# Kernel tuning notes

Measured on AMD Instinct MI355X. Metric: run time of the kernel, lower is better.

## Reference

```python
import math
import jax, jax.numpy as jnp
import numpy as np

B, V, F, H, W = 1, 2, 4, 16, 28
TPF = H * W            # 448 tokens per frame
VS = F * TPF           # 1792 tokens per view
TS = V * VS            # 3584 total tokens
DIM, NH = 1536, 12
HD = DIM // NH         # 128
EPS = 1e-6
SCALE = 1.0 / math.sqrt(HD)


def _rope_angle_table(max_len=1024):
    # Wan-style 3D rope: head_dim//2 = 64 channels split [22, 21, 21] for (f, h, w)
    parts = []
    for full in (44, 42, 42):
        inv = 1.0 / (10000.0 ** (np.arange(0, full, 2) / full))
        parts.append(np.outer(np.arange(max_len), inv))
    return np.concatenate(parts, axis=1).astype(np.float32)  # [max_len, 64]


def setup_inputs():
    key = jax.random.key(0)
    ks = jax.random.split(key, 6)
    p = lambda k, shp: 0.02 * jax.random.normal(k, shp, dtype=jnp.float32)
    return {
        "x": jax.random.normal(ks[0], (B, TS, DIM), dtype=jnp.float32),
        "freqs": jnp.asarray(_rope_angle_table()),
        "q_w": p(ks[1], (DIM, DIM)), "q_b": jnp.zeros((DIM,), jnp.float32),
        "k_w": p(ks[2], (DIM, DIM)), "k_b": jnp.zeros((DIM,), jnp.float32),
        "v_w": p(ks[3], (DIM, DIM)), "v_b": jnp.zeros((DIM,), jnp.float32),
        "o_w": p(ks[4], (DIM, DIM)), "o_b": jnp.zeros((DIM,), jnp.float32),
        "norm_q_w": jnp.ones((DIM,), jnp.float32),
        "norm_k_w": jnp.ones((DIM,), jnp.float32),
        "seq_lens": jnp.full((B,), TS, jnp.int32),
        "view_grid_sizes": jnp.broadcast_to(jnp.array([F, H, W], jnp.int32), (B, V, 3)),
        "view_seq_lens": jnp.full((B, V), VS, jnp.int32),
        "total_seq_lens": jnp.full((B,), TS, jnp.int32),
    }


def _rms_norm(x, w):
    x32 = x.astype(jnp.float32)
    y = x32 * jax.lax.rsqrt(jnp.mean(x32 * x32, axis=-1, keepdims=True) + EPS)
    return y.astype(x.dtype) * w


def _rope_angles(freqs):
    c = HD // 2                                   # 64
    s0, s1 = c - 2 * (c // 3), c // 3             # 22, 21
    af = jnp.broadcast_to(freqs[:F, None, None, :s0], (F, H, W, s0))
    ah = jnp.broadcast_to(freqs[None, :H, None, s0:s0 + s1], (F, H, W, s1))
    aw = jnp.broadcast_to(freqs[None, None, :W, s0 + s1:c], (F, H, W, c - s0 - s1))
    return jnp.concatenate([af, ah, aw], axis=-1).reshape(VS, c)  # [VS, 64]


def _apply_rope(x, ang):
    # x: [N, S, NH, HD]; pairs are (x[..., 2i], x[..., 2i+1]) as in view_as_complex
    cos = jnp.cos(ang)[None, :, None, :]
    sin = jnp.sin(ang)[None, :, None, :]
    xr = x.reshape(x.shape[:-1] + (HD // 2, 2))
    r0 = xr[..., 0] * cos - xr[..., 1] * sin
    r1 = xr[..., 0] * sin + xr[..., 1] * cos
    return jnp.stack([r0, r1], axis=-1).reshape(x.shape)


def _attn_lse(q, k, v):
    # q,k,v: [N, S, NH, HD] -> out [N, S, NH, HD], lse [N, S, NH]
    logits = jnp.einsum('bqhd,bkhd->bhqk', q, k) * SCALE
    lse = jax.nn.logsumexp(logits, axis=-1)       # [N, NH, Sq]
    p = jnp.exp(logits - lse[..., None])
    out = jnp.einsum('bhqk,bkhd->bqhd', p, v)
    return out, jnp.transpose(lse, (0, 2, 1))


def _forward(x, freqs, q_w, q_b, k_w, k_b, v_w, v_b, o_w, o_b, norm_q_w, norm_k_w):
    xv = x[:, :TS]
    q = _rms_norm(xv @ q_w.T + q_b, norm_q_w)
    k = _rms_norm(xv @ k_w.T + k_b, norm_k_w)
    v = xv @ v_w.T + v_b
    q = q.reshape(B * V, VS, NH, HD)
    k = k.reshape(B * V, VS, NH, HD)
    v = v.reshape(B * V, VS, NH, HD)
    ang = _rope_angles(freqs)
    q = _apply_rope(q, ang)
    k = _apply_rope(k, ang)
    # intra-view attention over the full view sequence
    out_i, lse_i = _attn_lse(q, k, v)
    # cross-view per-frame attention: swap the two views for K/V
    k_sw = k.reshape(B, V, F, TPF, NH, HD)[:, ::-1].reshape(B * V * F, TPF, NH, HD)
    v_sw = v.reshape(B, V, F, TPF, NH, HD)[:, ::-1].reshape(B * V * F, TPF, NH, HD)
    q_c = q.reshape(B * V * F, TPF, NH, HD)
    out_c, lse_c = _attn_lse(q_c, k_sw, v_sw)
    out_i = out_i.reshape(B, V, F, TPF, NH, HD)
    lse_i = lse_i.reshape(B, V, F, TPF, NH)
    out_c = out_c.reshape(B, V, F, TPF, NH, HD)
    lse_c = lse_c.reshape(B, V, F, TPF, NH)
    # online-softmax-style LSE merge of the two attention results
    lse_u = jnp.logaddexp(lse_i, lse_c)
    fused = (jnp.exp(lse_i - lse_u)[..., None] * out_i
             + jnp.exp(lse_c - lse_u)[..., None] * out_c)
    fused = fused.reshape(B, TS, DIM)
    return fused @ o_w.T + o_b


def reference(x, freqs, q_w, q_b, k_w, k_b, v_w, v_b, o_w, o_b, norm_q_w, norm_k_w,
              seq_lens, view_grid_sizes, view_seq_lens, total_seq_lens):
    del seq_lens, view_grid_sizes, view_seq_lens, total_seq_lens  # validated layout constants
    return _forward(x, freqs, q_w, q_b, k_w, k_b, v_w, v_b, o_w, o_b, norm_q_w, norm_k_w)
```

## Files before the change

kernel.cpp:

```cpp
#include <hip/hip_runtime.h>

#define TS 3584
#define VS 1792
#define TPF 448
#define NHEAD 12
#define HDIM 128
#define DMODEL 1536
#define QK_PRESCALE (0.08838834764831845f * 1.4426950408889634f)

typedef unsigned short u16;
typedef unsigned int u32;
typedef __attribute__((ext_vector_type(8))) short bf16x8;
typedef __attribute__((ext_vector_type(4))) float f32x4;

__device__ __forceinline__ float u2f(u32 u) { union { u32 u; float f; } c; c.u = u; return c.f; }
__device__ __forceinline__ float blo(u32 u) { return u2f(u << 16); }
__device__ __forceinline__ float bhi(u32 u) { return u2f(u & 0xffff0000u); }
__device__ __forceinline__ u16 f2b(float f) {
  union { float f; u32 u; } c; c.f = f;
  return (u16)((c.u + 0x7fffu + ((c.u >> 16) & 1u)) >> 16);
}

__device__ __forceinline__ float exp2fast(float x) {
#if __has_builtin(__builtin_amdgcn_exp2f)
  return __builtin_amdgcn_exp2f(x);
#else
  float r; asm("v_exp_f32 %0, %1" : "=v"(r) : "v"(x)); return r;
#endif
}

__device__ __forceinline__ void gl16(const u16* g, u16* l) {
  __builtin_amdgcn_global_load_lds(
      (const __attribute__((address_space(1))) void*)g,
      (__attribute__((address_space(3))) void*)l, 16, 0, 0);
}

__global__ __launch_bounds__(256) void convert_bf16(
    const float* __restrict__ x, const float* __restrict__ qw,
    const float* __restrict__ kw, const float* __restrict__ vw,
    const float* __restrict__ ow, u16* __restrict__ xb,
    u16* __restrict__ wqkv, u16* __restrict__ owb) {
  const int z = blockIdx.y;
  const float* src;
  u16* dst;
  int n8;
  if (z == 0)      { src = x;  dst = xb;  n8 = TS * DMODEL / 8; }
  else if (z == 4) { src = ow; dst = owb; n8 = DMODEL * DMODEL / 8; }
  else {
    src = (z == 1) ? qw : (z == 2) ? kw : vw;
    dst = wqkv + (size_t)(z - 1) * DMODEL * DMODEL;
    n8 = DMODEL * DMODEL / 8;
  }
  const int idx = blockIdx.x * 256 + threadIdx.x;
  if (idx >= n8) return;
  const float4 a = ((const float4*)src)[2 * idx];
  const float4 b = ((const float4*)src)[2 * idx + 1];
  uint4 o;
  o.x = (u32)f2b(a.x) | ((u32)f2b(a.y) << 16);
  o.y = (u32)f2b(a.z) | ((u32)f2b(a.w) << 16);
  o.z = (u32)f2b(b.x) | ((u32)f2b(b.y) << 16);
  o.w = (u32)f2b(b.z) | ((u32)f2b(b.w) << 16);
  ((uint4*)dst)[idx] = o;
}

template <bool QKV>
__global__ __launch_bounds__(256) void gemm_mfma(
    const u16* __restrict__ A, const u16* __restrict__ W,
    const float* __restrict__ b0, const float* __restrict__ b1,
    const float* __restrict__ b2,
    u16* __restrict__ o0, u16* __restrict__ o1, u16* __restrict__ o2,
    float* __restrict__ of) {
  __shared__ __align__(16) u16 Als[128 * 64];
  __shared__ __align__(16) u16 Bls[128 * 64];
  const int t = threadIdx.x;
  const int wave = t >> 6, lane = t & 63, col = lane & 15, quad = lane >> 4;
  const int m0 = blockIdx.y * 128, n0 = blockIdx.x * 128;
  const int wm = (wave & 1) * 64, wn = (wave >> 1) * 64;
  f32x4 acc[4][4];
#pragma unroll
  for (int i = 0; i < 4; ++i)
#pragma unroll
    for (int j = 0; j < 4; ++j) acc[i][j] = (f32x4){0.f, 0.f, 0.f, 0.f};

  for (int k0 = 0; k0 < DMODEL; k0 += 64) {
    __syncthreads();
#pragma unroll
    for (int i = 0; i < 4; ++i) {
      const int idx = t + i * 256;
      const int row = idx >> 3, ch = idx & 7;
      *(uint4*)&Als[row * 64 + ((ch ^ (row & 7)) * 8)] =
          *(const uint4*)(A + (size_t)(m0 + row) * DMODEL + k0 + ch * 8);
      *(uint4*)&Bls[row * 64 + ((ch ^ (row & 7)) * 8)] =
          *(const uint4*)(W + (size_t)(n0 + row) * DMODEL + k0 + ch * 8);
    }
    __syncthreads();
#pragma unroll
    for (int s = 0; s < 2; ++s) {
      bf16x8 af[4], bv[4];
#pragma unroll
      for (int i = 0; i < 4; ++i) {
        const int r = wm + i * 16 + col;
        af[i] = *(const bf16x8*)&Als[r * 64 + (((s * 4 + quad) ^ (r & 7)) * 8)];
      }
#pragma unroll
      for (int j = 0; j < 4; ++j) {
        const int r = wn + j * 16 + col;
        bv[j] = *(const bf16x8*)&Bls[r * 64 + (((s * 4 + quad) ^ (r & 7)) * 8)];
      }
#pragma unroll
      for (int i = 0; i < 4; ++i)
#pragma unroll
        for (int j = 0; j < 4; ++j)
          acc[i][j] = __builtin_amdgcn_mfma_f32_16x16x32_bf16(af[i], bv[j], acc[i][j], 0, 0, 0);
    }
  }

#pragma unroll
  for (int j = 0; j < 4; ++j) {
    const int ng = n0 + wn + j * 16 + col;
    if constexpr (QKV) {
      const int sec = ng / DMODEL;
      const int nn = ng - sec * DMODEL;
      u16* dst = sec == 0 ? o0 : (sec == 1 ? o1 : o2);
      const float bias = sec == 0 ? b0[nn] : (sec == 1 ? b1[nn] : b2[nn]);
#pragma unroll
      for (int i = 0; i < 4; ++i) {
        const int mb = m0 + wm + i * 16 + quad * 4;
#pragma unroll
        for (int r = 0; r < 4; ++r)
          dst[(size_t)(mb + r) * DMODEL + nn] = f2b(acc[i][j][r] + bias);
      }
    } else {
      const float bias = b0[ng];
#pragma unroll
      for (int i = 0; i < 4; ++i) {
        const int mb = m0 + wm + i * 16 + quad * 4;
#pragma unroll
        for (int r = 0; r < 4; ++r)
          of[(size_t)(mb + r) * DMODEL + ng] = acc[i][j][r] + bias;
      }
    }
  }
}

__global__ __launch_bounds__(256) void rmsnorm_rope(
    u16* qbuf, u16* kbuf, const float* __restrict__ freqs,
    const float* __restrict__ nqw, const float* __restrict__ nkw) {
  const int tok = blockIdx.x;
  u32* row = (u32*)((blockIdx.y == 0 ? qbuf : kbuf) + (size_t)tok * DMODEL);
  const float* w = blockIdx.y == 0 ? nqw : nkw;
  const int t = threadIdx.x;
  const u32 u0 = row[t], u1 = row[t + 256], u2 = row[t + 512];
  float px[3] = { blo(u0), blo(u1), blo(u2) };
  float py[3] = { bhi(u0), bhi(u1), bhi(u2) };
  float ss = px[0] * px[0] + py[0] * py[0] + px[1] * px[1] + py[1] * py[1] +
             px[2] * px[2] + py[2] * py[2];
#pragma unroll
  for (int off = 32; off; off >>= 1) ss += __shfl_xor(ss, off);
  __shared__ float red[4];
  if ((t & 63) == 0) red[t >> 6] = ss;
  __syncthreads();
  float rstd = rsqrtf((red[0] + red[1] + red[2] + red[3]) * (1.0f / DMODEL) + 1e-6f);
  if (blockIdx.y == 0) rstd *= QK_PRESCALE;
  const int p = tok % VS;
  const int fi = p / TPF, rem = p % TPF, hi = rem / 28, wi = rem % 28;
#pragma unroll
  for (int jj = 0; jj < 3; ++jj) {
    const int pj = t + jj * 256;
    const int i = pj & 63;
    const int prow = (i < 22) ? fi : ((i < 43) ? hi : wi);
    const float ang = freqs[prow * 64 + i];
    float sn, cs;
    sincosf(ang, &sn, &cs);
    const float a = px[jj] * rstd * w[2 * pj], b = py[jj] * rstd * w[2 * pj + 1];
    row[pj] = (u32)f2b(a * cs - b * sn) | ((u32)f2b(a * sn + b * cs) << 16);
  }
}

__global__ __launch_bounds__(128) void transpose_v(
    const u16* __restrict__ v, u16* __restrict__ vt) {
  __shared__ __align__(16) u16 T[128 * 128];
  const int h = blockIdx.y;
  const int t0 = blockIdx.x * 128;
  const int t = threadIdx.x;
#pragma unroll
  for (int i = 0; i < 16; ++i) {
    int idx = t + i * 128;
    int tok = idx >> 4, hd8 = idx & 15;
    *(uint4*)&T[tok * 128 + ((hd8 ^ (tok & 7)) * 8)] =
        *(const uint4*)(v + (size_t)(t0 + tok) * DMODEL + h * HDIM + hd8 * 8);
  }
  __syncthreads();
  const int hb = t >> 3;
#pragma unroll
  for (int half = 0; half < 2; ++half) {
    const int tb = (t & 7) + half * 8;
    uint4 M[8];
#pragma unroll
    for (int r = 0; r < 8; ++r)
      M[r] = *(const uint4*)&T[(tb * 8 + r) * 128 + ((hb ^ r) * 8)];
    uint4 O[8];
#pragma unroll
    for (int c2 = 0; c2 < 4; ++c2) {
      const u32* A = (const u32*)&M[2 * c2];
      const u32* Bp = (const u32*)&M[2 * c2 + 1];
#pragma unroll
      for (int jh = 0; jh < 4; ++jh) {
        u32 a = A[jh], b = Bp[jh];
        ((u32*)&O[2 * jh])[c2] = (a & 0xffffu) | (b << 16);
        ((u32*)&O[2 * jh + 1])[c2] = (a >> 16) | (b & 0xffff0000u);
      }
    }
#pragma unroll
    for (int j = 0; j < 8; ++j)
      *(uint4*)(vt + (size_t)(h * HDIM + hb * 8 + j) * TS + t0 + tb * 8) = O[j];
  }
}

__global__ __launch_bounds__(256) void attn_mfma(
    const u16* __restrict__ q, const u16* __restrict__ k,
    const u16* __restrict__ vt, u16* __restrict__ fused) {
  __shared__ __align__(16) u16 Kls[2 * 64 * 128];
  __shared__ __align__(16) u16 Vls[64 * 128];
  const int t = threadIdx.x;
  const int wave = t >> 6, lane = t & 63;
  const int col = lane & 15, quad = lane >> 4;
  const int d = blockIdx.y * 56 + blockIdx.x;
  const int wk = (d & 7) * 84 + (d >> 3);
  const int h = wk / 56;
  const int qb = wk - h * 56;
  const int q0 = qb * 64;
  const int vview = q0 / VS;
  const int fidx = (q0 % VS) / TPF;
  const int base0 = vview * VS;
  const int base1 = (1 - vview) * VS + fidx * TPF;
  const int jmp = base1 - (base0 + 27 * 64);

  bf16x8 qfrag[4];
#pragma unroll
  for (int c = 0; c < 4; ++c)
    qfrag[c] = *(const bf16x8*)(q + (size_t)(q0 + wave * 16 + col) * DMODEL +
                                h * HDIM + ((c * 4 + quad) << 3));

  const u16* ksrc[4];
  const u16* vsrc[4];
#pragma unroll
  for (int j = 0; j < 4; ++j) {
    const int ci = (wave * 4 + j) * 64 + lane;
    const int key = ci >> 4, c = ci & 15;
    const int krow = key & 31;
    const int k4 = ((krow >> 1) & 12) | (krow & 3);
    ksrc[j] = k + (size_t)(base0 + key) * DMODEL + h * HDIM + ((c ^ k4) << 3);
    const int sub = ci >> 9, hd = (ci >> 2) & 127, sl = ci & 3;
    vsrc[j] = vt + (size_t)(h * HDIM + hd) * TS + base0 + sub * 32 +
              ((sl ^ (hd & 3)) << 3);
  }
  const int r0 = ((col & 12) << 1) | (col & 3);
  int koffu[4];
#pragma unroll
  for (int c = 0; c < 4; ++c) koffu[c] = r0 * 128 + (((c * 4 + quad) ^ col) << 3);
  const int voffu = col * 32 + ((quad ^ (col & 3)) << 3);

#pragma unroll
  for (int j = 0; j < 4; ++j)
    gl16(ksrc[j], &Kls[(wave * 4 + j) * 512]);
  int tK = 0, tV = 0;
  {
    const int dK = (tK == 27) ? jmp : 64; ++tK;
#pragma unroll
    for (int j = 0; j < 4; ++j) ksrc[j] += (ptrdiff_t)dK * DMODEL;
  }

  f32x4 accO[8];
#pragma unroll
  for (int c = 0; c < 8; ++c) accO[c] = (f32x4){0.f, 0.f, 0.f, 0.f};
  float m_run = -1e30f, l_run = 0.f;

#define AITER(CUR, LAST)                                                       \
  do {                                                                         \
    _Pragma("unroll") for (int j = 0; j < 4; ++j)                              \
        gl16(vsrc[j], &Vls[(wave * 4 + j) * 512]);                             \
    {                                                                          \
      const int dV = (tV == 27) ? jmp : 64; ++tV;                              \
      _Pragma("unroll") for (int j = 0; j < 4; ++j) vsrc[j] += (ptrdiff_t)dV;  \
    }                                                                          \
    if (!(LAST)) {                                                             \
      _Pragma("unroll") for (int j = 0; j < 4; ++j)                            \
          gl16(ksrc[j], &Kls[((CUR) ^ 1) * 8192 + (wave * 4 + j) * 512]);      \
      const int dK = (tK == 27) ? jmp : 64; ++tK;                              \
      _Pragma("unroll") for (int j = 0; j < 4; ++j)                            \
          ksrc[j] += (ptrdiff_t)dK * DMODEL;                                   \
    }                                                                          \
    asm volatile("s_waitcnt vmcnt(%0)" ::"i"((LAST) ? 4 : 8) : "memory");      \
    __builtin_amdgcn_s_barrier();                                              \
    asm volatile("" ::: "memory");                                             \
    f32x4 s0 = (f32x4){0.f, 0.f, 0.f, 0.f}, s1 = s0, s2 = s0, s3 = s0;        \
    __builtin_amdgcn_s_setprio(1);                                             \
    _Pragma("unroll") for (int c = 0; c < 4; ++c) {                            \
      bf16x8 ka0 = *(const bf16x8*)&Kls[(CUR)*8192 + koffu[c]];                \
      bf16x8 ka1 = *(const bf16x8*)&Kls[(CUR)*8192 + koffu[c] + 512];          \
      s0 = __builtin_amdgcn_mfma_f32_16x16x32_bf16(ka0, qfrag[c], s0, 0, 0, 0);\
      s1 = __builtin_amdgcn_mfma_f32_16x16x32_bf16(ka1, qfrag[c], s1, 0, 0, 0);\
    }                                                                          \
    _Pragma("unroll") for (int c = 0; c < 4; ++c) {                            \
      bf16x8 kb0 = *(const bf16x8*)&Kls[(CUR)*8192 + 4096 + koffu[c]];         \
      bf16x8 kb1 = *(const bf16x8*)&Kls[(CUR)*8192 + 4096 + koffu[c] + 512];   \
      s2 = __builtin_amdgcn_mfma_f32_16x16x32_bf16(kb0, qfrag[c], s2, 0, 0, 0);\
      s3 = __builtin_amdgcn_mfma_f32_16x16x32_bf16(kb1, qfrag[c], s3, 0, 0, 0);\
    }                                                                          \
    __builtin_amdgcn_s_setprio(0);                                             \
    float lmax = fmaxf(fmaxf(fmaxf(s0[0], s0[1]), fmaxf(s0[2], s0[3])),        \
                       fmaxf(fmaxf(s1[0], s1[1]), fmaxf(s1[2], s1[3])));       \
    lmax = fmaxf(lmax, fmaxf(fmaxf(fmaxf(s2[0], s2[1]), fmaxf(s2[2], s2[3])),  \
                             fmaxf(fmaxf(s3[0], s3[1]), fmaxf(s3[2], s3[3]))));\
    lmax = fmaxf(lmax, __shfl_xor(lmax, 16));                                  \
    lmax = fmaxf(lmax, __shfl_xor(lmax, 32));                                  \
    if (__any(lmax > m_run + 8.f)) {                                           \
      const float mnew = fmaxf(m_run, lmax);                                   \
      const float alpha = exp2fast(m_run - mnew);                              \
      _Pragma("unroll") for (int c = 0; c < 8; ++c) {                          \
        accO[c][0] *= alpha; accO[c][1] *= alpha;                              \
        accO[c][2] *= alpha; accO[c][3] *= alpha;                              \
      }                                                                        \
      l_run *= alpha;                                                          \
      m_run = mnew;                                                            \
    }                                                                          \
    float ps = 0.f;                                                            \
    _Pragma("unroll") for (int r = 0; r < 4; ++r) {                            \
      s0[r] = exp2fast(s0[r] - m_run); s1[r] = exp2fast(s1[r] - m_run);        \
      s2[r] = exp2fast(s2[r] - m_run); s3[r] = exp2fast(s3[r] - m_run);        \
      ps += (s0[r] + s1[r]) + (s2[r] + s3[r]);                                 \
    }                                                                          \
    union { u32 w[4]; bf16x8 v; } pu0, pu1;                                    \
    asm("v_cvt_pk_bf16_f32 %0, %1, %2" : "=v"(pu0.w[0]) : "v"(s0[0]), "v"(s0[1])); \
    asm("v_cvt_pk_bf16_f32 %0, %1, %2" : "=v"(pu0.w[1]) : "v"(s0[2]), "v"(s0[3])); \
    asm("v_cvt_pk_bf16_f32 %0, %1, %2" : "=v"(pu0.w[2]) : "v"(s1[0]), "v"(s1[1])); \
    asm("v_cvt_pk_bf16_f32 %0, %1, %2" : "=v"(pu0.w[3]) : "v"(s1[2]), "v"(s1[3])); \
    asm("v_cvt_pk_bf16_f32 %0, %1, %2" : "=v"(pu1.w[0]) : "v"(s2[0]), "v"(s2[1])); \
    asm("v_cvt_pk_bf16_f32 %0, %1, %2" : "=v"(pu1.w[1]) : "v"(s2[2]), "v"(s2[3])); \
    asm("v_cvt_pk_bf16_f32 %0, %1, %2" : "=v"(pu1.w[2]) : "v"(s3[0]), "v"(s3[1])); \
    asm("v_cvt_pk_bf16_f32 %0, %1, %2" : "=v"(pu1.w[3]) : "v"(s3[2]), "v"(s3[3])); \
    asm volatile("s_waitcnt vmcnt(%0)" ::"i"((LAST) ? 0 : 4) : "memory");      \
    __builtin_amdgcn_s_barrier();                                              \
    asm volatile("" ::: "memory");                                             \
    __builtin_amdgcn_s_setprio(1);                                             \
    _Pragma("unroll") for (int c = 0; c < 8; ++c) {                            \
      bf16x8 va0 = *(const bf16x8*)&Vls[voffu + c * 512];                      \
      accO[c] = __builtin_amdgcn_mfma_f32_16x16x32_bf16(va0, pu0.v, accO[c], 0, 0, 0); \
    }                                                                          \
    _Pragma("unroll") for (int c = 0; c < 8; ++c) {                            \
      bf16x8 va1 = *(const bf16x8*)&Vls[4096 + voffu + c * 512];               \
      accO[c] = __builtin_amdgcn_mfma_f32_16x16x32_bf16(va1, pu1.v, accO[c], 0, 0, 0); \
    }                                                                          \
    __builtin_amdgcn_s_setprio(0);                                             \
    ps += __shfl_xor(ps, 16);                                                  \
    ps += __shfl_xor(ps, 32);                                                  \
    l_run += ps;                                                               \
    if (!(LAST)) {                                                             \
      asm volatile("" ::: "memory");                                           \
      __builtin_amdgcn_s_barrier();                                            \
    }                                                                          \
  } while (0)

  for (int tt = 0; tt < 17; ++tt) {
    AITER(0, false);
    AITER(1, false);
  }
  AITER(0, true);
#undef AITER

  const float inv = 1.0f / l_run;
  const int token = q0 + wave * 16 + col;
  u16* orow = fused + (size_t)token * DMODEL + h * HDIM;
#pragma unroll
  for (int c = 0; c < 8; ++c) {
    uint2 ov;
    ov.x = (u32)f2b(accO[c][0] * inv) | ((u32)f2b(accO[c][1] * inv) << 16);
    ov.y = (u32)f2b(accO[c][2] * inv) | ((u32)f2b(accO[c][3] * inv) << 16);
    *(uint2*)(orow + c * 16 + quad * 4) = ov;
  }
}

extern "C" void kernel_launch(void* const* d_in, const int* in_sizes, int n_in,
                              void* d_out, int out_size, void* d_ws, size_t ws_size,
                              hipStream_t stream) {
  (void)in_sizes; (void)n_in; (void)out_size; (void)ws_size;
  const float* x   = (const float*)d_in[0];
  const float* fr  = (const float*)d_in[1];
  const float* qw  = (const float*)d_in[2];
  const float* qb  = (const float*)d_in[3];
  const float* kw  = (const float*)d_in[4];
  const float* kb  = (const float*)d_in[5];
  const float* vw  = (const float*)d_in[6];
  const float* vb  = (const float*)d_in[7];
  const float* ow  = (const float*)d_in[8];
  const float* ob  = (const float*)d_in[9];
  const float* nqw = (const float*)d_in[10];
  const float* nkw = (const float*)d_in[11];

  u16* qf   = (u16*)d_ws;
  u16* vf   = qf + (size_t)TS * DMODEL;
  u16* xb   = vf + (size_t)TS * DMODEL;
  u16* wqkv = xb + (size_t)TS * DMODEL;
  u16* owb  = wqkv + (size_t)3 * DMODEL * DMODEL;
  u16* kf   = (u16*)d_out;
  u16* vtb  = (u16*)d_out + (size_t)TS * DMODEL;

  convert_bf16<<<dim3(TS * DMODEL / 8 / 256, 5), dim3(256), 0, stream>>>(
      x, qw, kw, vw, ow, xb, wqkv, owb);
  gemm_mfma<true><<<dim3(3 * DMODEL / 128, TS / 128), dim3(256), 0, stream>>>(
      xb, wqkv, qb, kb, vb, qf, kf, vf, nullptr);
  rmsnorm_rope<<<dim3(TS, 2), dim3(256), 0, stream>>>(qf, kf, fr, nqw, nkw);
  transpose_v<<<dim3(TS / 128, NHEAD), dim3(128), 0, stream>>>(vf, vtb);
  attn_mfma<<<dim3(TS / 64, NHEAD), dim3(256), 0, stream>>>(qf, kf, vtb, qf);
  gemm_mfma<false><<<dim3(DMODEL / 128, TS / 128), dim3(256), 0, stream>>>(
      qf, owb, ob, nullptr, nullptr, nullptr, nullptr, nullptr, (float*)d_out);
}
```

Before: 360.2 us.

## Shrink attention KV tiles to 32 with double-buffered K and V, async GEMM loads

The attention kernel now processes 32-key tiles and double-buffers both K and V in shared memory, issuing the next tile's K and V loads together. This replaces the 64-key tile with double-buffered K and a single V buffer, and removes one barrier per iteration. The GEMM switches its global-to-shared staging to direct async loads (gl16) using precomputed swizzled pointers, and remaps workgroups in a strided order for better cache locality. Smaller tiles mean twice as many iterations and barriers, and less MFMA work per synchronisation.

```diff
diff --git a/kernel.cpp b/kernel.cpp
--- a/kernel.cpp
+++ b/kernel.cpp
@@ -74,8 +74,24 @@
   __shared__ __align__(16) u16 Bls[128 * 64];
   const int t = threadIdx.x;
   const int wave = t >> 6, lane = t & 63, col = lane & 15, quad = lane >> 4;
-  const int m0 = blockIdx.y * 128, n0 = blockIdx.x * 128;
+  const int nwg = gridDim.x * gridDim.y;
+  const int dlin = blockIdx.y * gridDim.x + blockIdx.x;
+  const int wk = (dlin & 7) * (nwg >> 3) + (dlin >> 3);
+  const int by = wk / gridDim.x, bx = wk - by * gridDim.x;
+  const int m0 = by * 128, n0 = bx * 128;
   const int wm = (wave & 1) * 64, wn = (wave >> 1) * 64;
+
+  const int srow = lane >> 3;
+  const int sch = (lane & 7) ^ srow;
+  const u16* pA[4];
+  const u16* pB[4];
+#pragma unroll
+  for (int i = 0; i < 4; ++i) {
+    const int r = i * 32 + wave * 8 + srow;
+    pA[i] = A + (size_t)(m0 + r) * DMODEL + sch * 8;
+    pB[i] = W + (size_t)(n0 + r) * DMODEL + sch * 8;
+  }
+
   f32x4 acc[4][4];
 #pragma unroll
   for (int i = 0; i < 4; ++i)
@@ -86,12 +102,8 @@
     __syncthreads();
 #pragma unroll
     for (int i = 0; i < 4; ++i) {
-      const int idx = t + i * 256;
-      const int row = idx >> 3, ch = idx & 7;
-      *(uint4*)&Als[row * 64 + ((ch ^ (row & 7)) * 8)] =
-          *(const uint4*)(A + (size_t)(m0 + row) * DMODEL + k0 + ch * 8);
-      *(uint4*)&Bls[row * 64 + ((ch ^ (row & 7)) * 8)] =
-          *(const uint4*)(W + (size_t)(n0 + row) * DMODEL + k0 + ch * 8);
+      gl16(pA[i] + k0, &Als[i * 2048 + wave * 512]);
+      gl16(pB[i] + k0, &Bls[i * 2048 + wave * 512]);
     }
     __syncthreads();
 #pragma unroll
@@ -220,8 +232,8 @@
 __global__ __launch_bounds__(256) void attn_mfma(
     const u16* __restrict__ q, const u16* __restrict__ k,
     const u16* __restrict__ vt, u16* __restrict__ fused) {
-  __shared__ __align__(16) u16 Kls[2 * 64 * 128];
-  __shared__ __align__(16) u16 Vls[64 * 128];
+  __shared__ __align__(16) u16 Kls[2 * 32 * 128];
+  __shared__ __align__(16) u16 Vls[2 * 128 * 32];
   const int t = threadIdx.x;
   const int wave = t >> 6, lane = t & 63;
   const int col = lane & 15, quad = lane >> 4;
@@ -234,7 +246,7 @@
   const int fidx = (q0 % VS) / TPF;
   const int base0 = vview * VS;
   const int base1 = (1 - vview) * VS + fidx * TPF;
-  const int jmp = base1 - (base0 + 27 * 64);
+  const int jmpd = base1 - base0 - 1760;
 
   bf16x8 qfrag[4];
 #pragma unroll
@@ -242,18 +254,16 @@
     qfrag[c] = *(const bf16x8*)(q + (size_t)(q0 + wave * 16 + col) * DMODEL +
                                 h * HDIM + ((c * 4 + quad) << 3));
 
-  const u16* ksrc[4];
-  const u16* vsrc[4];
-#pragma unroll
-  for (int j = 0; j < 4; ++j) {
-    const int ci = (wave * 4 + j) * 64 + lane;
+  const u16* ksrc[2];
+  const u16* vsrc[2];
+#pragma unroll
+  for (int j = 0; j < 2; ++j) {
+    const int ci = (wave * 2 + j) * 64 + lane;
     const int key = ci >> 4, c = ci & 15;
-    const int krow = key & 31;
-    const int k4 = ((krow >> 1) & 12) | (krow & 3);
+    const int k4 = ((key >> 1) & 12) | (key & 3);
     ksrc[j] = k + (size_t)(base0 + key) * DMODEL + h * HDIM + ((c ^ k4) << 3);
-    const int sub = ci >> 9, hd = (ci >> 2) & 127, sl = ci & 3;
-    vsrc[j] = vt + (size_t)(h * HDIM + hd) * TS + base0 + sub * 32 +
-              ((sl ^ (hd & 3)) << 3);
+    const int hd = ci >> 2, sl = ci & 3;
+    vsrc[j] = vt + (size_t)(h * HDIM + hd) * TS + base0 + ((sl ^ (hd & 3)) << 3);
   }
   const int r0 = ((col & 12) << 1) | (col & 3);
   int koffu[4];
@@ -262,14 +272,13 @@
   const int voffu = col * 32 + ((quad ^ (col & 3)) << 3);
 
 #pragma unroll
-  for (int j = 0; j < 4; ++j)
-    gl16(ksrc[j], &Kls[(wave * 4 + j) * 512]);
-  int tK = 0, tV = 0;
-  {
-    const int dK = (tK == 27) ? jmp : 64; ++tK;
-#pragma unroll
-    for (int j = 0; j < 4; ++j) ksrc[j] += (ptrdiff_t)dK * DMODEL;
-  }
+  for (int j = 0; j < 2; ++j) {
+    gl16(ksrc[j], &Kls[(wave * 2 + j) * 512]);
+    gl16(vsrc[j], &Vls[(wave * 2 + j) * 512]);
+  }
+  int ts = 1;
+#pragma unroll
+  for (int j = 0; j < 2; ++j) { ksrc[j] += 32 * DMODEL; vsrc[j] += 32; }
 
   f32x4 accO[8];
 #pragma unroll
@@ -278,41 +287,30 @@
 
 #define AITER(CUR, LAST)                                                       \
   do {                                                                         \
-    _Pragma("unroll") for (int j = 0; j < 4; ++j)                              \
-        gl16(vsrc[j], &Vls[(wave * 4 + j) * 512]);                             \
-    {                                                                          \
-      const int dV = (tV == 27) ? jmp : 64; ++tV;                              \
-      _Pragma("unroll") for (int j = 0; j < 4; ++j) vsrc[j] += (ptrdiff_t)dV;  \
-    }                                                                          \
     if (!(LAST)) {                                                             \
-      _Pragma("unroll") for (int j = 0; j < 4; ++j)                            \
-          gl16(ksrc[j], &Kls[((CUR) ^ 1) * 8192 + (wave * 4 + j) * 512]);      \
-      const int dK = (tK == 27) ? jmp : 64; ++tK;                              \
-      _Pragma("unroll") for (int j = 0; j < 4; ++j)                            \
-          ksrc[j] += (ptrdiff_t)dK * DMODEL;                                   \
-    }                                                                          \
-    asm volatile("s_waitcnt vmcnt(%0)" ::"i"((LAST) ? 4 : 8) : "memory");      \
+      _Pragma("unroll") for (int j = 0; j < 2; ++j) {                          \
+        gl16(ksrc[j], &Kls[((CUR) ^ 1) * 4096 + (wave * 2 + j) * 512]);        \
+        gl16(vsrc[j], &Vls[((CUR) ^ 1) * 4096 + (wave * 2 + j) * 512]);        \
+      }                                                                        \
+      const int dd = (ts == 55) ? jmpd : 32; ++ts;                             \
+      _Pragma("unroll") for (int j = 0; j < 2; ++j) {                          \
+        ksrc[j] += (ptrdiff_t)dd * DMODEL; vsrc[j] += dd;                      \
+      }                                                                        \
+    }                                                                          \
+    asm volatile("s_waitcnt vmcnt(%0)" ::"i"((LAST) ? 0 : 4) : "memory");      \
     __builtin_amdgcn_s_barrier();                                              \
     asm volatile("" ::: "memory");                                             \
-    f32x4 s0 = (f32x4){0.f, 0.f, 0.f, 0.f}, s1 = s0, s2 = s0, s3 = s0;        \
+    f32x4 s0 = (f32x4){0.f, 0.f, 0.f, 0.f}, s1 = s0;                           \
     __builtin_amdgcn_s_setprio(1);                                             \
     _Pragma("unroll") for (int c = 0; c < 4; ++c) {                            \
-      bf16x8 ka0 = *(const bf16x8*)&Kls[(CUR)*8192 + koffu[c]];                \
-      bf16x8 ka1 = *(const bf16x8*)&Kls[(CUR)*8192 + koffu[c] + 512];          \
+      bf16x8 ka0 = *(const bf16x8*)&Kls[(CUR) * 4096 + koffu[c]];              \
+      bf16x8 ka1 = *(const bf16x8*)&Kls[(CUR) * 4096 + koffu[c] + 512];        \
       s0 = __builtin_amdgcn_mfma_f32_16x16x32_bf16(ka0, qfrag[c], s0, 0, 0, 0);\
       s1 = __builtin_amdgcn_mfma_f32_16x16x32_bf16(ka1, qfrag[c], s1, 0, 0, 0);\
-    }                                                                          \
-    _Pragma("unroll") for (int c = 0; c < 4; ++c) {                            \
-      bf16x8 kb0 = *(const bf16x8*)&Kls[(CUR)*8192 + 4096 + koffu[c]];         \
-      bf16x8 kb1 = *(const bf16x8*)&Kls[(CUR)*8192 + 4096 + koffu[c] + 512];   \
-      s2 = __builtin_amdgcn_mfma_f32_16x16x32_bf16(kb0, qfrag[c], s2, 0, 0, 0);\
-      s3 = __builtin_amdgcn_mfma_f32_16x16x32_bf16(kb1, qfrag[c], s3, 0, 0, 0);\
     }                                                                          \
     __builtin_amdgcn_s_setprio(0);                                             \
     float lmax = fmaxf(fmaxf(fmaxf(s0[0], s0[1]), fmaxf(s0[2], s0[3])),        \
                        fmaxf(fmaxf(s1[0], s1[1]), fmaxf(s1[2], s1[3])));       \
-    lmax = fmaxf(lmax, fmaxf(fmaxf(fmaxf(s2[0], s2[1]), fmaxf(s2[2], s2[3])),  \
-                             fmaxf(fmaxf(s3[0], s3[1]), fmaxf(s3[2], s3[3]))));\
     lmax = fmaxf(lmax, __shfl_xor(lmax, 16));                                  \
     lmax = fmaxf(lmax, __shfl_xor(lmax, 32));                                  \
     if (__any(lmax > m_run + 8.f)) {                                           \
@@ -328,45 +326,35 @@
     float ps = 0.f;                                                            \
     _Pragma("unroll") for (int r = 0; r < 4; ++r) {                            \
       s0[r] = exp2fast(s0[r] - m_run); s1[r] = exp2fast(s1[r] - m_run);        \
-      s2[r] = exp2fast(s2[r] - m_run); s3[r] = exp2fast(s3[r] - m_run);        \
-      ps += (s0[r] + s1[r]) + (s2[r] + s3[r]);                                 \
-    }                                                                          \
-    union { u32 w[4]; bf16x8 v; } pu0, pu1;                                    \
-    asm("v_cvt_pk_bf16_f32 %0, %1, %2" : "=v"(pu0.w[0]) : "v"(s0[0]), "v"(s0[1])); \
-    asm("v_cvt_pk_bf16_f32 %0, %1, %2" : "=v"(pu0.w[1]) : "v"(s0[2]), "v"(s0[3])); \
-    asm("v_cvt_pk_bf16_f32 %0, %1, %2" : "=v"(pu0.w[2]) : "v"(s1[0]), "v"(s1[1])); \
-    asm("v_cvt_pk_bf16_f32 %0, %1, %2" : "=v"(pu0.w[3]) : "v"(s1[2]), "v"(s1[3])); \
-    asm("v_cvt_pk_bf16_f32 %0, %1, %2" : "=v"(pu1.w[0]) : "v"(s2[0]), "v"(s2[1])); \
-    asm("v_cvt_pk_bf16_f32 %0, %1, %2" : "=v"(pu1.w[1]) : "v"(s2[2]), "v"(s2[3])); \
-    asm("v_cvt_pk_bf16_f32 %0, %1, %2" : "=v"(pu1.w[2]) : "v"(s3[0]), "v"(s3[1])); \
-    asm("v_cvt_pk_bf16_f32 %0, %1, %2" : "=v"(pu1.w[3]) : "v"(s3[2]), "v"(s3[3])); \
-    asm volatile("s_waitcnt vmcnt(%0)" ::"i"((LAST) ? 0 : 4) : "memory");      \
-    __builtin_amdgcn_s_barrier();                                              \
-    asm volatile("" ::: "memory");                                             \
+      ps += s0[r] + s1[r];                                                     \
+    }                                                                          \
+    union { u32 w[4]; bf16x8 v; } pu;                                          \
+    asm("v_cvt_pk_bf16_f32 %0, %1, %2" : "=v"(pu.w[0]) : "v"(s0[0]), "v"(s0[1])); \
+    asm("v_cvt_pk_bf16_f32 %0, %1, %2" : "=v"(pu.w[1]) : "v"(s0[2]), "v"(s0[3])); \
+    asm("v_cvt_pk_bf16_f32 %0, %1, %2" : "=v"(pu.w[2]) : "v"(s1[0]), "v"(s1[1])); \
+    asm("v_cvt_pk_bf16_f32 %0, %1, %2" : "=v"(pu.w[3]) : "v"(s1[2]), "v"(s1[3])); \
     __builtin_amdgcn_s_setprio(1);                                             \
     _Pragma("unroll") for (int c = 0; c < 8; ++c) {                            \
-      bf16x8 va0 = *(const bf16x8*)&Vls[voffu + c * 512];                      \
-      accO[c] = __builtin_amdgcn_mfma_f32_16x16x32_bf16(va0, pu0.v, accO[c], 0, 0, 0); \
-    }                                                                          \
-    _Pragma("unroll") for (int c = 0; c < 8; ++c) {                            \
-      bf16x8 va1 = *(const bf16x8*)&Vls[4096 + voffu + c * 512];               \
-      accO[c] = __builtin_amdgcn_mfma_f32_16x16x32_bf16(va1, pu1.v, accO[c], 0, 0, 0); \
+      bf16x8 va = *(const bf16x8*)&Vls[(CUR) * 4096 + voffu + c * 512];        \
+      accO[c] = __builtin_amdgcn_mfma_f32_16x16x32_bf16(va, pu.v, accO[c], 0, 0, 0); \
     }                                                                          \
     __builtin_amdgcn_s_setprio(0);                                             \
+    if (!(LAST)) {                                                             \
+      asm volatile("" ::: "memory");                                           \
+      __builtin_amdgcn_s_barrier();                                            \
+      asm volatile("" ::: "memory");                                           \
+    }                                                                          \
     ps += __shfl_xor(ps, 16);                                                  \
     ps += __shfl_xor(ps, 32);                                                  \
     l_run += ps;                                                               \
-    if (!(LAST)) {                                                             \
-      asm volatile("" ::: "memory");                                           \
-      __builtin_amdgcn_s_barrier();                                            \
-    }                                                                          \
   } while (0)
 
-  for (int tt = 0; tt < 17; ++tt) {
+  for (int tt = 0; tt < 34; ++tt) {
     AITER(0, false);
     AITER(1, false);
   }
-  AITER(0, true);
+  AITER(0, false);
+  AITER(1, true);
 #undef AITER
 
   const float inv = 1.0f / l_run;
```

Result: faster. 321.6 us (-10.7%).
